# Optimization experiments

Hardware: AMD Instinct MI355X
Metric: run time of the kernel (lower is better)

The kernel has to match this reference:

```python
import jax, jax.numpy as jnp
import numpy as np

DIM = 2048
N_HEADS = 16
HEAD_DIM = DIM // N_HEADS  # 128
B, T = 8, 1024


def setup_inputs() -> dict:
    key = jax.random.key(0)
    ks = jax.random.split(key, 5)
    s_in = 1.0 / np.sqrt(DIM)
    return {
        "x": jax.random.normal(ks[0], (B, T, DIM), dtype=jnp.float32),
        "W_qkv": jax.random.uniform(ks[1], (DIM + 2 * HEAD_DIM, DIM), dtype=jnp.float32, minval=-s_in, maxval=s_in),
        "b_qkv": jax.random.uniform(ks[2], (DIM + 2 * HEAD_DIM,), dtype=jnp.float32, minval=-s_in, maxval=s_in),
        "W_out": jax.random.uniform(ks[3], (DIM, DIM), dtype=jnp.float32, minval=-s_in, maxval=s_in),
        "b_out": jax.random.uniform(ks[4], (DIM,), dtype=jnp.float32, minval=-s_in, maxval=s_in),
    }


def reference(x, W_qkv, b_qkv, W_out, b_out):
    Bx, Tx, D = x.shape
    H, hd = N_HEADS, HEAD_DIM
    qkv = x @ W_qkv.T + b_qkv                      # [B,T,D+2*hd]
    q = qkv[:, :, :D].reshape(Bx, Tx, H, hd).transpose(0, 2, 1, 3)  # [B,H,T,hd]
    k = qkv[:, :, D:D + hd]                        # [B,T,hd] (shared head)
    v = qkv[:, :, D + hd:]                         # [B,T,hd]
    # torch repeat(1,1,H).view(B,T,H,hd) duplicates the single KV head -> broadcast instead
    scores = jnp.einsum('bhtd,bsd->bhts', q, k) / jnp.sqrt(jnp.asarray(hd, x.dtype))
    causal = jnp.tril(jnp.ones((Tx, Tx), dtype=bool))
    scores = jnp.where(causal[None, None], scores, jnp.asarray(-jnp.inf, x.dtype))
    att = jax.nn.softmax(scores, axis=-1)          # [B,H,T,T]
    out = jnp.einsum('bhts,bsd->bhtd', att, v)     # [B,H,T,hd]
    out = out.transpose(0, 2, 1, 3).reshape(Bx, Tx, D)
    return out @ W_out.T + b_out
```

## Files before the change

### kernel.cpp

```cpp
#include <hip/hip_runtime.h>
#include <hip/hip_bf16.h>
#include <math.h>
#include <stdint.h>

#define DIM 2048
#define NH 16
#define HD 128
#define BB 8
#define TT 1024
#define NROW (BB*TT)
#define QKVD (DIM + 2*HD)

typedef unsigned short u16;
typedef unsigned int u32;
typedef float f32x4 __attribute__((ext_vector_type(4)));
typedef u32 u32x4 __attribute__((ext_vector_type(4)));
typedef __bf16 bf16x8 __attribute__((ext_vector_type(8)));

#define QSCALE_LOG2E (0.08838834764831845f * 1.4426950408889634f)

__device__ inline u16 f2bf(float f) {
  u32 u = __builtin_bit_cast(u32, f);
  u += 0x7FFF + ((u >> 16) & 1);
  return (u16)(u >> 16);
}

__device__ inline u32 cvt_pk_bf16(float lo, float hi) {
  u32 d;
  asm("v_cvt_pk_bf16_f32 %0, %1, %2" : "=v"(d) : "v"(lo), "v"(hi));
  return d;
}

__device__ inline void gload_lds16(const void* g, void* l) {
  __builtin_amdgcn_global_load_lds(
      (const __attribute__((address_space(1))) void*)g,
      (__attribute__((address_space(3))) void*)l,
      16, 0, 0);
}

__global__ void cvt_f32_bf16(const float* __restrict__ in, u16* __restrict__ out, int n4) {
  int i = blockIdx.x * blockDim.x + threadIdx.x;
  int st = gridDim.x * blockDim.x;
  for (; i < n4; i += st) {
    float4 v = reinterpret_cast<const float4*>(in)[i];
    ushort4 o;
    o.x = f2bf(v.x); o.y = f2bf(v.y); o.z = f2bf(v.z); o.w = f2bf(v.w);
    reinterpret_cast<ushort4*>(out)[i] = o;
  }
}

template<bool OUT_BF16, bool WRITE_VT>
__global__ __launch_bounds__(256, 3) void gemm_nt(
    const u16* __restrict__ A, const u16* __restrict__ Bm,
    const float* __restrict__ bias, void* __restrict__ Cout,
    u16* __restrict__ vT, int K, int Mcols)
{
  __shared__ __align__(16) u16 sbuf[3][8192];
  const int tid = threadIdx.x;
  const int w = tid >> 6, l = tid & 63;
  const int wm = w >> 1, wn = w & 1;
  const int rl = l & 15, gl = l >> 4;
  const int rowBase = blockIdx.x * 128;
  const int colBase = blockIdx.y * 128;

  const int rT = tid >> 2;
  const int t4 = tid & 3;
  const int cswE = (t4 * 8) ^ (((rT >> 1) & 3) << 3);
  const u16* aSrc0 = A  + (size_t)(rowBase + rT) * K + cswE;
  const u16* bSrc0 = Bm + (size_t)(colBase + rT) * K + cswE;
  const size_t rowSk = (size_t)64 * K;

  auto STAGE = [&](int kt) {
    u16* base = &sbuf[kt % 3][0];
    const int k0 = kt * 32;
    gload_lds16(aSrc0 + k0,         base + (size_t)tid * 8);
    gload_lds16(aSrc0 + rowSk + k0, base + 2048 + (size_t)tid * 8);
    gload_lds16(bSrc0 + k0,         base + 4096 + (size_t)tid * 8);
    gload_lds16(bSrc0 + rowSk + k0, base + 4096 + 2048 + (size_t)tid * 8);
  };

  int aOff[4], bOff[4];
#pragma unroll
  for (int f = 0; f < 4; ++f) {
    int ra = wm * 64 + f * 16 + rl;
    aOff[f] = ra * 32 + ((gl * 8) ^ (((ra >> 1) & 3) << 3));
    int rb = wn * 64 + f * 16 + rl;
    bOff[f] = 4096 + rb * 32 + ((gl * 8) ^ (((rb >> 1) & 3) << 3));
  }

  f32x4 acc[4][4] = {};

#define GEMM_BODY(KT)                                                          \
  {                                                                            \
    __builtin_amdgcn_sched_barrier(0);                                         \
    __builtin_amdgcn_s_barrier();                                              \
    const u16* base = &sbuf[(KT) % 3][0];                                      \
    bf16x8 af[4], bf[4];                                                       \
    _Pragma("unroll")                                                          \
    for (int f = 0; f < 4; ++f) af[f] = *(const bf16x8*)(base + aOff[f]);      \
    _Pragma("unroll")                                                          \
    for (int f = 0; f < 4; ++f) bf[f] = *(const bf16x8*)(base + bOff[f]);      \
    asm volatile("s_waitcnt lgkmcnt(0)" ::: "memory");                         \
    __builtin_amdgcn_sched_barrier(0);                                         \
    __builtin_amdgcn_s_barrier();                                              \
    __builtin_amdgcn_s_setprio(1);                                             \
    _Pragma("unroll")                                                          \
    for (int fm = 0; fm < 4; ++fm)                                             \
      _Pragma("unroll")                                                        \
      for (int fn = 0; fn < 4; ++fn)                                           \
        acc[fm][fn] = __builtin_amdgcn_mfma_f32_16x16x32_bf16(af[fm], bf[fn],  \
                                                              acc[fm][fn], 0, 0, 0); \
    __builtin_amdgcn_s_setprio(0);                                             \
  }

  const int NT = K >> 5;
  STAGE(0);
  STAGE(1);

  for (int kt = 0; kt < NT - 2; ++kt) {
    STAGE(kt + 2);
    asm volatile("s_waitcnt vmcnt(8)" ::: "memory");
    GEMM_BODY(kt);
  }
  asm volatile("s_waitcnt vmcnt(4)" ::: "memory");
  GEMM_BODY(NT - 2);
  asm volatile("s_waitcnt vmcnt(0)" ::: "memory");
  GEMM_BODY(NT - 1);
#undef GEMM_BODY

  float bv[4];
#pragma unroll
  for (int fn = 0; fn < 4; ++fn) bv[fn] = bias[colBase + wn*64 + fn*16 + rl];

#pragma unroll
  for (int fm = 0; fm < 4; ++fm) {
#pragma unroll
    for (int fn = 0; fn < 4; ++fn) {
      const int col = colBase + wn*64 + fn*16 + rl;
#pragma unroll
      for (int r = 0; r < 4; ++r) {
        const int row = rowBase + wm*64 + fm*16 + gl*4 + r;
        float v = acc[fm][fn][r] + bv[fn];
        if (WRITE_VT && col >= DIM + HD) {
          int d = col - (DIM + HD);
          int b = row >> 10, t = row & 1023;
          vT[((size_t)(b*HD + d) << 10) + t] = f2bf(v);
        }
        float vs = (WRITE_VT && col < DIM) ? v * QSCALE_LOG2E : v;
        if (OUT_BF16) ((u16*)Cout)[(size_t)row*Mcols + col] = f2bf(vs);
        else          ((float*)Cout)[(size_t)row*Mcols + col] = vs;
      }
    }
  }
}

__global__ __launch_bounds__(512, 4) void mqa_attn(
    const u16* __restrict__ qkv, const u16* __restrict__ vT,
    u16* __restrict__ attout)
{
  __shared__ char lds[65536];

  const int tid = threadIdx.x;
  const int wid = tid >> 6, l = tid & 63;
  const int rl = l & 15, gl = l >> 4;
  const int qb = (int)gridDim.x - 1 - (int)blockIdx.x;
  const int b = blockIdx.y >> 4, h = blockIdx.y & 15;
  const int qrow0 = qb*128 + wid*16;
  const int diag = qrow0 >> 6;
  const int itmax = 2*qb + 1;

  const u16* kbase = qkv + (size_t)b*TT*QKVD + DIM;
  const u16* vbase = vT + ((size_t)b*HD << 10);

  auto STAGE = [&](int buf, int s0) {
    char* kl = lds + buf*32768;
    char* vl = kl + 16384;
#pragma unroll
    for (int i = 0; i < 2; ++i) {
      int L = (i*8 + wid)*1024 + l*16;
      int s = L >> 8, kb = (L & 255) ^ ((s & 7) << 4);
      gload_lds16(kbase + (size_t)(s0 + s)*QKVD + (kb >> 1), kl + (i*8 + wid)*1024);
      int d = L >> 7, sb = (L & 127) ^ ((d & 7) << 4);
      gload_lds16(vbase + ((size_t)d << 10) + s0 + (sb >> 1), vl + (i*8 + wid)*1024);
    }
  };

  STAGE(0, 0);
  asm volatile("" ::: "memory");

  bf16x8 qf[4];
  {
    const u16* qp = qkv + (size_t)(b*TT + qrow0 + rl)*QKVD + h*HD + gl*8;
#pragma unroll
    for (int kk = 0; kk < 4; ++kk) qf[kk] = *(const bf16x8*)(qp + kk*32);
  }

  f32x4 accO[8] = {};
  float mrow = -INFINITY, lrow = 0.f;
  const int tg = qrow0 + rl;
  const int addrA = (((gl & 1) * 2) * 16 + rl) * 4;
  const int addrB = addrA + 64;
  const bool hiSel = (gl >= 2);

  for (int it = 0; it <= itmax; ++it) {
    if (it < itmax) {
      STAGE((it + 1) & 1, (it + 1) << 6);
      asm volatile("s_waitcnt vmcnt(4)" ::: "memory");
    } else {
      asm volatile("s_waitcnt vmcnt(0)" ::: "memory");
    }
    __builtin_amdgcn_s_barrier();

    if (it <= diag) {
      const char* kl = lds + (it & 1)*32768;
      const char* vl = kl + 16384;

      f32x4 sc[4] = {};
      __builtin_amdgcn_s_setprio(1);
#pragma unroll
      for (int fs = 0; fs < 4; ++fs) {
        const int s = fs*16 + rl;
#pragma unroll
        for (int kkd = 0; kkd < 4; ++kkd) {
          bf16x8 kf = *(const bf16x8*)(kl + ((s*256 + kkd*64 + gl*16) ^ ((s & 7) << 4)));
          sc[fs] = __builtin_amdgcn_mfma_f32_16x16x32_bf16(kf, qf[kkd], sc[fs], 0, 0, 0);
        }
      }
      __builtin_amdgcn_s_setprio(0);

      if (it == diag) {
        const int s0 = it << 6;
#pragma unroll
        for (int fs = 0; fs < 4; ++fs)
#pragma unroll
          for (int r = 0; r < 4; ++r) {
            int sg = s0 + fs*16 + gl*4 + r;
            if (sg > tg) sc[fs][r] = -INFINITY;
          }
      }

      float mx = -INFINITY;
#pragma unroll
      for (int fs = 0; fs < 4; ++fs)
        mx = fmaxf(mx, fmaxf(fmaxf(sc[fs][0], sc[fs][1]), fmaxf(sc[fs][2], sc[fs][3])));
      mx = fmaxf(mx, __shfl_xor(mx, 16));
      mx = fmaxf(mx, __shfl_xor(mx, 32));

      if (!__all(mx <= mrow + 8.f)) {
        float mnew = fmaxf(mrow, mx);
        float rr = __builtin_amdgcn_exp2f(mrow - mnew);
#pragma unroll
        for (int fd = 0; fd < 8; ++fd)
#pragma unroll
          for (int r = 0; r < 4; ++r) accO[fd][r] *= rr;
        lrow *= rr;
        mrow = mnew;
      }

      float ps = 0.f;
#pragma unroll
      for (int fs = 0; fs < 4; ++fs)
#pragma unroll
        for (int r = 0; r < 4; ++r) {
          float p = __builtin_amdgcn_exp2f(sc[fs][r] - mrow);
          sc[fs][r] = p;
          ps += p;
        }
      ps += __shfl_xor(ps, 16);
      ps += __shfl_xor(ps, 32);
      lrow += ps;

      u32 pw[4][2];
#pragma unroll
      for (int fs = 0; fs < 4; ++fs) {
        pw[fs][0] = cvt_pk_bf16(sc[fs][0], sc[fs][1]);
        pw[fs][1] = cvt_pk_bf16(sc[fs][2], sc[fs][3]);
      }
      u32x4 bw[2];
#pragma unroll
      for (int kk = 0; kk < 2; ++kk)
#pragma unroll
        for (int w = 0; w < 4; ++w) {
          int addr = (w < 2) ? addrA : addrB;
          u32 lo = __builtin_amdgcn_ds_bpermute(addr, (int)pw[2*kk + 0][w & 1]);
          u32 hi = __builtin_amdgcn_ds_bpermute(addr, (int)pw[2*kk + 1][w & 1]);
          bw[kk][w] = hiSel ? hi : lo;
        }

      __builtin_amdgcn_s_setprio(1);
#pragma unroll
      for (int kk = 0; kk < 2; ++kk) {
        bf16x8 pb = __builtin_bit_cast(bf16x8, bw[kk]);
#pragma unroll
        for (int fd = 0; fd < 8; ++fd) {
          const int d = fd*16 + rl;
          bf16x8 vf = *(const bf16x8*)(vl + ((d*128 + kk*64 + gl*16) ^ ((d & 7) << 4)));
          accO[fd] = __builtin_amdgcn_mfma_f32_16x16x32_bf16(vf, pb, accO[fd], 0, 0, 0);
        }
      }
      __builtin_amdgcn_s_setprio(0);
    }

    __builtin_amdgcn_s_barrier();
  }

  const float inv = 1.0f / lrow;
  u16* outp = attout + (size_t)(b*TT + tg)*DIM + h*HD;
#pragma unroll
  for (int fd = 0; fd < 8; ++fd) {
    ushort4 o;
    o.x = f2bf(accO[fd][0] * inv);
    o.y = f2bf(accO[fd][1] * inv);
    o.z = f2bf(accO[fd][2] * inv);
    o.w = f2bf(accO[fd][3] * inv);
    *(ushort4*)(outp + fd*16 + gl*4) = o;
  }
}

extern "C" void kernel_launch(void* const* d_in, const int* in_sizes, int n_in,
                              void* d_out, int out_size, void* d_ws, size_t ws_size,
                              hipStream_t stream) {
  const float* x    = (const float*)d_in[0];
  const float* Wqkv = (const float*)d_in[1];
  const float* bqkv = (const float*)d_in[2];
  const float* Wout = (const float*)d_in[3];
  const float* bout = (const float*)d_in[4];

  char* ws = (char*)d_ws;
  u16* xb    = (u16*)(ws);
  u16* wqb   = (u16*)(ws + 33554432);
  u16* qkvb  = (u16*)(ws + 33554432 + 9437184);
  u16* vtb   = (u16*)(ws + 33554432 + 9437184 + 37748736);
  u16* attb  = xb;
  u16* woutb = wqb;

  cvt_f32_bf16<<<2048, 256, 0, stream>>>(x,    xb,  NROW*DIM/4);
  cvt_f32_bf16<<<2048, 256, 0, stream>>>(Wqkv, wqb, QKVD*DIM/4);

  dim3 g1(NROW/128, QKVD/128);
  gemm_nt<true, true><<<g1, 256, 0, stream>>>(xb, wqb, bqkv, qkvb, vtb, DIM, QKVD);

  cvt_f32_bf16<<<2048, 256, 0, stream>>>(Wout, woutb, DIM*DIM/4);

  dim3 ga(TT/128, BB*NH);
  mqa_attn<<<ga, 512, 0, stream>>>(qkvb, vtb, attb);

  dim3 g2(NROW/128, DIM/128);
  gemm_nt<false, false><<<g2, 256, 0, stream>>>(attb, woutb, bout, d_out, nullptr, DIM, DIM);
}
```

Measured before the change: 305.9 us.

## Halve attention KV tile to 32 keys to double occupancy

The attention kernel now stages 32-key K/V tiles instead of 64, which halves LDS use to 32KB and raises the launch bound to 8 blocks per CU. Staging, the swizzle patterns, the causal diagonal index and the P·V loop are rewritten for the smaller tile, so each iteration does a single bpermute/MFMA pass. The goal is more resident waves to hide latency and finer causal skipping. The cost is twice as many barriers and online-softmax rescale checks per key span, plus tighter register limits that could cause spills.

```diff
diff --git a/kernel.cpp b/kernel.cpp
--- a/kernel.cpp
+++ b/kernel.cpp
@@ -154,11 +154,11 @@
   }
 }
 
-__global__ __launch_bounds__(512, 4) void mqa_attn(
+__global__ __launch_bounds__(512, 8) void mqa_attn(
     const u16* __restrict__ qkv, const u16* __restrict__ vT,
     u16* __restrict__ attout)
 {
-  __shared__ char lds[65536];
+  __shared__ char lds[32768];
 
   const int tid = threadIdx.x;
   const int wid = tid >> 6, l = tid & 63;
@@ -166,23 +166,21 @@
   const int qb = (int)gridDim.x - 1 - (int)blockIdx.x;
   const int b = blockIdx.y >> 4, h = blockIdx.y & 15;
   const int qrow0 = qb*128 + wid*16;
-  const int diag = qrow0 >> 6;
-  const int itmax = 2*qb + 1;
+  const int diag = qrow0 >> 5;
+  const int itmax = 4*qb + 3;
 
   const u16* kbase = qkv + (size_t)b*TT*QKVD + DIM;
   const u16* vbase = vT + ((size_t)b*HD << 10);
 
+  const int ks = tid >> 4;
+  const int kchunk = (tid & 15) ^ (ks & 7);
+  const int vd = tid >> 2;
+  const int vchunk = (tid & 3) ^ ((vd >> 1) & 3);
+
   auto STAGE = [&](int buf, int s0) {
-    char* kl = lds + buf*32768;
-    char* vl = kl + 16384;
-#pragma unroll
-    for (int i = 0; i < 2; ++i) {
-      int L = (i*8 + wid)*1024 + l*16;
-      int s = L >> 8, kb = (L & 255) ^ ((s & 7) << 4);
-      gload_lds16(kbase + (size_t)(s0 + s)*QKVD + (kb >> 1), kl + (i*8 + wid)*1024);
-      int d = L >> 7, sb = (L & 127) ^ ((d & 7) << 4);
-      gload_lds16(vbase + ((size_t)d << 10) + s0 + (sb >> 1), vl + (i*8 + wid)*1024);
-    }
+    char* base = lds + buf*16384;
+    gload_lds16(kbase + (size_t)(s0 + ks)*QKVD + kchunk*8, base + tid*16);
+    gload_lds16(vbase + ((size_t)vd << 10) + s0 + vchunk*8, base + 8192 + tid*16);
   };
 
   STAGE(0, 0);
@@ -204,21 +202,22 @@
 
   for (int it = 0; it <= itmax; ++it) {
     if (it < itmax) {
-      STAGE((it + 1) & 1, (it + 1) << 6);
-      asm volatile("s_waitcnt vmcnt(4)" ::: "memory");
+      STAGE((it + 1) & 1, (it + 1) << 5);
+      asm volatile("s_waitcnt vmcnt(2)" ::: "memory");
     } else {
       asm volatile("s_waitcnt vmcnt(0)" ::: "memory");
     }
     __builtin_amdgcn_s_barrier();
 
     if (it <= diag) {
-      const char* kl = lds + (it & 1)*32768;
-      const char* vl = kl + 16384;
-
-      f32x4 sc[4] = {};
+      const char* kl = lds + (it & 1)*16384;
+      const char* vl = kl + 8192;
+      const int s0 = it << 5;
+
+      f32x4 sc[2] = {};
       __builtin_amdgcn_s_setprio(1);
 #pragma unroll
-      for (int fs = 0; fs < 4; ++fs) {
+      for (int fs = 0; fs < 2; ++fs) {
         const int s = fs*16 + rl;
 #pragma unroll
         for (int kkd = 0; kkd < 4; ++kkd) {
@@ -229,9 +228,8 @@
       __builtin_amdgcn_s_setprio(0);
 
       if (it == diag) {
-        const int s0 = it << 6;
-#pragma unroll
-        for (int fs = 0; fs < 4; ++fs)
+#pragma unroll
+        for (int fs = 0; fs < 2; ++fs)
 #pragma unroll
           for (int r = 0; r < 4; ++r) {
             int sg = s0 + fs*16 + gl*4 + r;
@@ -239,10 +237,8 @@
           }
       }
 
-      float mx = -INFINITY;
-#pragma unroll
-      for (int fs = 0; fs < 4; ++fs)
-        mx = fmaxf(mx, fmaxf(fmaxf(sc[fs][0], sc[fs][1]), fmaxf(sc[fs][2], sc[fs][3])));
+      float mx = fmaxf(fmaxf(fmaxf(sc[0][0], sc[0][1]), fmaxf(sc[0][2], sc[0][3])),
+                       fmaxf(fmaxf(sc[1][0], sc[1][1]), fmaxf(sc[1][2], sc[1][3])));
       mx = fmaxf(mx, __shfl_xor(mx, 16));
       mx = fmaxf(mx, __shfl_xor(mx, 32));
 
@@ -259,7 +255,7 @@
 
       float ps = 0.f;
 #pragma unroll
-      for (int fs = 0; fs < 4; ++fs)
+      for (int fs = 0; fs < 2; ++fs)
 #pragma unroll
         for (int r = 0; r < 4; ++r) {
           float p = __builtin_amdgcn_exp2f(sc[fs][r] - mrow);
@@ -270,33 +266,28 @@
       ps += __shfl_xor(ps, 32);
       lrow += ps;
 
-      u32 pw[4][2];
-#pragma unroll
-      for (int fs = 0; fs < 4; ++fs) {
+      u32 pw[2][2];
+#pragma unroll
+      for (int fs = 0; fs < 2; ++fs) {
         pw[fs][0] = cvt_pk_bf16(sc[fs][0], sc[fs][1]);
         pw[fs][1] = cvt_pk_bf16(sc[fs][2], sc[fs][3]);
       }
-      u32x4 bw[2];
-#pragma unroll
-      for (int kk = 0; kk < 2; ++kk)
-#pragma unroll
-        for (int w = 0; w < 4; ++w) {
-          int addr = (w < 2) ? addrA : addrB;
-          u32 lo = __builtin_amdgcn_ds_bpermute(addr, (int)pw[2*kk + 0][w & 1]);
-          u32 hi = __builtin_amdgcn_ds_bpermute(addr, (int)pw[2*kk + 1][w & 1]);
-          bw[kk][w] = hiSel ? hi : lo;
-        }
+      u32x4 bw;
+#pragma unroll
+      for (int w = 0; w < 4; ++w) {
+        int addr = (w < 2) ? addrA : addrB;
+        u32 lo = __builtin_amdgcn_ds_bpermute(addr, (int)pw[0][w & 1]);
+        u32 hi = __builtin_amdgcn_ds_bpermute(addr, (int)pw[1][w & 1]);
+        bw[w] = hiSel ? hi : lo;
+      }
+      bf16x8 pb = __builtin_bit_cast(bf16x8, bw);
 
       __builtin_amdgcn_s_setprio(1);
 #pragma unroll
-      for (int kk = 0; kk < 2; ++kk) {
-        bf16x8 pb = __builtin_bit_cast(bf16x8, bw[kk]);
-#pragma unroll
-        for (int fd = 0; fd < 8; ++fd) {
-          const int d = fd*16 + rl;
-          bf16x8 vf = *(const bf16x8*)(vl + ((d*128 + kk*64 + gl*16) ^ ((d & 7) << 4)));
-          accO[fd] = __builtin_amdgcn_mfma_f32_16x16x32_bf16(vf, pb, accO[fd], 0, 0, 0);
-        }
+      for (int fd = 0; fd < 8; ++fd) {
+        const int d = fd*16 + rl;
+        bf16x8 vf = *(const bf16x8*)(vl + d*64 + ((gl ^ ((d >> 1) & 3)) << 4));
+        accO[fd] = __builtin_amdgcn_mfma_f32_16x16x32_bf16(vf, pb, accO[fd], 0, 0, 0);
       }
       __builtin_amdgcn_s_setprio(0);
     }
```

After: 499.2 us. 1.63x slower.
